# Optimization experiments

Hardware: AMD Instinct MI355X
Metric: run time of the kernel (lower is better)

## Reference

```python
import jax, jax.numpy as jnp
import numpy as np
import math

B, L, I, H = 32, 2048, 64, 512
HALF = H // 2
DT = 0.05
RHO = 0.99
INPUT_SCALING = 1.0
STD = 1.0
GAMMA_MIN, GAMMA_MAX = 0.5, 1.0
EPS_MIN, EPS_MAX = 0.5, 1.0


def setup_inputs() -> dict:
    key = jax.random.key(0)
    ks = jax.random.split(key, 7)
    x = jax.random.normal(ks[0], (B, L, I), dtype=jnp.float32)
    x2h = jax.random.uniform(ks[1], (I, H), dtype=jnp.float32) * INPUT_SCALING
    h2h = 2.0 * (2.0 * jax.random.uniform(ks[2], (H, H), dtype=jnp.float32) - 1.0)
    # spectral_norm_scaling: rescale so largest singular value == rho
    h2h = h2h * (RHO / jnp.linalg.norm(h2h, ord=2))
    bias = (2.0 * jax.random.uniform(ks[3], (H,), dtype=jnp.float32) - 1.0) * INPUT_SCALING
    gamma = jax.random.uniform(ks[4], (H,), dtype=jnp.float32) * (GAMMA_MAX - GAMMA_MIN) + GAMMA_MIN
    epsilon = jax.random.uniform(ks[5], (H,), dtype=jnp.float32) * (EPS_MAX - EPS_MIN) + EPS_MIN
    # RandomFourierFeature: W_sin = W_cos, shape [half_dim, in_dim]
    W_rff = jax.random.normal(ks[6], (HALF, H), dtype=jnp.float32) * STD
    return {"x": x, "x2h": x2h, "h2h": h2h, "bias": bias,
            "gamma": gamma, "epsilon": epsilon, "W_rff": W_rff}


def _run(x, x2h, h2h, bias, gamma, epsilon, W_rff):
    b = x.shape[0]
    inv_sqrt_half = 1.0 / math.sqrt(HALF)

    def step(carry, xt):
        hy, hz, zsum = carry
        pre = jnp.tanh(xt @ x2h + hy @ h2h + bias)          # [B,H]
        hz = hz + DT * (pre - gamma * hy - epsilon * hz)
        hy = hy + DT * hz
        wx = hy @ W_rff.T                                   # [B,HALF]
        z = jnp.concatenate([jnp.cos(wx), jnp.sin(wx)], axis=-1) * inv_sqrt_half
        return (hy, hz, zsum + z), None

    hy0 = jnp.zeros((b, H), dtype=x.dtype)
    hz0 = jnp.zeros((b, H), dtype=x.dtype)
    zsum0 = jnp.zeros((b, H), dtype=x.dtype)
    (hy, hz, zsum), _ = jax.lax.scan(step, (hy0, hz0, zsum0), jnp.swapaxes(x, 0, 1))
    mu = zsum / x.shape[1]  # mean over time of per-step RFF states
    return mu, hy


def reference(x, x2h, h2h, bias, gamma, epsilon, W_rff):
    return _run(x, x2h, h2h, bias, gamma, epsilon, W_rff)
```

## Files before the change

### kernel.cpp

```cpp
#include <hip/hip_runtime.h>
#include <math.h>

#define Bz 32
#define Lz 2048
#define Iz 64
#define Hz 512
#define HALFz 256
#define DTz 0.05f
#define NMEM 8
#define TPB 512

#define FMA4(P, S, W) do { (P).x = fmaf((S), (W).x, (P).x); (P).y = fmaf((S), (W).y, (P).y); \
                           (P).z = fmaf((S), (W).z, (P).z); (P).w = fmaf((S), (W).w, (P).w); } while(0)

__global__ __launch_bounds__(TPB, 2) void coesn_l2(
    const float* __restrict__ x, const float* __restrict__ x2h,
    const float* __restrict__ h2h, const float* __restrict__ bias,
    const float* __restrict__ gam, const float* __restrict__ eps,
    const float* __restrict__ W_rff, unsigned long long* __restrict__ gbuf,
    float* __restrict__ out) {
  __shared__ __align__(16) float hyf[2][Hz];
  __shared__ __align__(16) float xb[2][Iz];
  __shared__ __align__(16) float part[NMEM][64];

  const int b    = blockIdx.x & 31;
  const int m    = blockIdx.x >> 5;
  const int u    = threadIdx.x;
  const int c0   = m * 64;
  const int ksl  = u >> 4;
  const int cg   = u & 15;
  const int wv   = u >> 6;
  const int lane = u & 63;
  const int rloc = u >> 4;
  const int kseg = u & 15;

  float4 wreg[16];
  #pragma unroll
  for (int k = 0; k < 16; ++k)
    wreg[k] = *(const float4*)(h2h + (size_t)(ksl * 16 + k) * Hz + c0 + 4 * cg);
  float4 xreg[2];
  #pragma unroll
  for (int j = 0; j < 2; ++j)
    xreg[j] = *(const float4*)(x2h + (size_t)(ksl * 2 + j) * Hz + c0 + 4 * cg);
  float wr[32];
  {
    const float* wp = W_rff + (size_t)(m * 32 + rloc) * Hz + kseg * 32;
    #pragma unroll
    for (int j = 0; j < 32; ++j) wr[j] = wp[j];
  }

  float hy = 0.f, hz = 0.f, bu = 0.f, gu = 0.f, eu = 0.f;
  if (u < 64) { bu = bias[c0 + u]; gu = gam[c0 + u]; eu = eps[c0 + u]; }
  hyf[0][u] = 0.f;
  if (u < 16) ((float4*)xb[0])[u] = ((const float4*)(x + (size_t)b * Lz * Iz))[u];
  float zc = 0.f, zs = 0.f;
  __syncthreads();

  auto rff_acc = [&](const float* hsrc) {
    float acc = 0.f;
    #pragma unroll
    for (int i = 0; i < 8; ++i) {
      int q = kseg * 8 + i;
      float4 h4 = ((const float4*)hsrc)[q ^ ((q >> 3) & 7)];
      acc = fmaf(h4.x, wr[4 * i], acc);
      acc = fmaf(h4.y, wr[4 * i + 1], acc);
      acc = fmaf(h4.z, wr[4 * i + 2], acc);
      acc = fmaf(h4.w, wr[4 * i + 3], acc);
    }
    acc += __shfl_xor(acc, 1); acc += __shfl_xor(acc, 2);
    acc += __shfl_xor(acc, 4); acc += __shfl_xor(acc, 8);
    float sv, cv;
    __sincosf(acc, &sv, &cv);
    zc += cv; zs += sv;
  };

  for (int t = 0; t < Lz; ++t) {
    const int cur = t & 1, nxt = cur ^ 1;

    float hv[16];
    #pragma unroll
    for (int j = 0; j < 4; ++j) {
      int q = ksl * 4 + j;
      float4 h4 = ((const float4*)hyf[cur])[q ^ ((q >> 3) & 7)];
      hv[4 * j] = h4.x; hv[4 * j + 1] = h4.y; hv[4 * j + 2] = h4.z; hv[4 * j + 3] = h4.w;
    }
    float4 p = make_float4(0.f, 0.f, 0.f, 0.f);
    #pragma unroll
    for (int k = 0; k < 16; ++k) FMA4(p, hv[k], wreg[k]);
    {
      const float* xcur = xb[cur];
      FMA4(p, xcur[ksl * 2], xreg[0]);
      FMA4(p, xcur[ksl * 2 + 1], xreg[1]);
    }
    if (u < 16 && t + 1 < Lz)
      ((float4*)xb[nxt])[u] =
          ((const float4*)(x + ((size_t)b * Lz + (t + 1)) * Iz))[u];
    p.x += __shfl_xor(p.x, 16); p.y += __shfl_xor(p.y, 16);
    p.z += __shfl_xor(p.z, 16); p.w += __shfl_xor(p.w, 16);
    p.x += __shfl_xor(p.x, 32); p.y += __shfl_xor(p.y, 32);
    p.z += __shfl_xor(p.z, 32); p.w += __shfl_xor(p.w, 32);
    if (lane < 16) ((float4*)part[wv])[lane] = p;
    __syncthreads();

    const unsigned tag = (unsigned)(t + 1);
    unsigned long long* A = gbuf + ((size_t)nxt * Bz + b) * Hz;

    if (u < 64) {
      float s = 0.f;
      #pragma unroll
      for (int w = 0; w < 8; ++w) s += part[w][u];
      s += bu;
      float e2 = __expf(s + s);
      float pre = 1.f - 2.f * __builtin_amdgcn_rcpf(e2 + 1.f);
      float hzn = fmaf(DTz, pre - gu * hy - eu * hz, hz);
      hy = fmaf(DTz, hzn, hy);
      hz = hzn;
      unsigned bits = __float_as_uint(hy);
      unsigned ax = (bits & 0xffff0000u) | tag;
      unsigned ay = (bits << 16) | tag;
      *(volatile unsigned long long*)(A + c0 + u) =
          ((unsigned long long)ay << 32) | ax;
      unsigned* Bd = (unsigned*)(A + c0 + u);
      __hip_atomic_store(Bd, ax, __ATOMIC_RELAXED, __HIP_MEMORY_SCOPE_AGENT);
      __hip_atomic_store(Bd + 1, ay, __ATOMIC_RELAXED, __HIP_MEMORY_SCOPE_AGENT);
      int q = (c0 + u) >> 2;
      hyf[nxt][(q ^ ((q >> 3) & 7)) * 4 + (u & 3)] = hy;
    }

    if (t > 0) rff_acc(hyf[cur]);

    if (wv != m) {
      unsigned ax, ay; int it = 0;
      for (;;) {
        unsigned long long v = *(volatile const unsigned long long*)(A + u);
        ax = (unsigned)v; ay = (unsigned)(v >> 32);
        if (!(((ax ^ tag) | (ay ^ tag)) & 0xffffu)) break;
        if (it >= 4) {
          const unsigned* Bd = (const unsigned*)(A + u);
          ax = __hip_atomic_load(Bd, __ATOMIC_RELAXED, __HIP_MEMORY_SCOPE_AGENT);
          ay = __hip_atomic_load(Bd + 1, __ATOMIC_RELAXED, __HIP_MEMORY_SCOPE_AGENT);
          if (!(((ax ^ tag) | (ay ^ tag)) & 0xffffu)) break;
        }
        if (++it > (1 << 20)) break;
      }
      int q = u >> 2;
      hyf[nxt][(q ^ ((q >> 3) & 7)) * 4 + (u & 3)] =
          __uint_as_float((ax & 0xffff0000u) | (ay >> 16));
    }
    __syncthreads();
  }

  rff_acc(hyf[0]);

  if (u < 64) out[(size_t)Bz * Hz + (size_t)b * Hz + c0 + u] = hy;
  if (kseg == 0) {
    const float sc = 0.0625f / 2048.f;
    out[(size_t)b * Hz + m * 32 + rloc] = zc * sc;
    out[(size_t)b * Hz + HALFz + m * 32 + rloc] = zs * sc;
  }
}

__global__ __launch_bounds__(512) void coesn_scan_fb(
    const float* __restrict__ x, const float* __restrict__ x2h,
    const float* __restrict__ h2h, const float* __restrict__ bias,
    const float* __restrict__ gam, const float* __restrict__ eps,
    const float* __restrict__ W_rff, float* __restrict__ out) {
  const int b = blockIdx.x;
  const int u = threadIdx.x;
  __shared__ __align__(16) float hy_lds[Hz];
  __shared__ __align__(16) float x_lds[Iz];
  __shared__ float4 part[4][128];
  __shared__ float wx_lds[HALFz];

  float hy = 0.f, hz = 0.f, zsum = 0.f;
  const float bu = bias[u];
  const float gu = gam[u];
  const float eu = eps[u];

  const int kq = u >> 7;
  const int g  = u & 127;
  const int jj = u >> 2;
  const int ks = u & 3;

  const float4* __restrict__ H4 = (const float4*)h2h;
  const float4* __restrict__ X2 = (const float4*)x2h;
  const float4* __restrict__ W4 = (const float4*)W_rff;
  const float4* __restrict__ XG = (const float4*)x;
  const float4* hy4 = (const float4*)hy_lds;

  hy_lds[u] = 0.f;
  if (u < 16) ((float4*)x_lds)[u] = XG[(long)b * Lz * 16 + u];
  __syncthreads();

  for (int t = 0; t < Lz; ++t) {
    float4 p = make_float4(0.f, 0.f, 0.f, 0.f);
    {
      const float4* hp = (const float4*)&hy_lds[kq << 7];
      #pragma unroll 8
      for (int k4 = 0; k4 < 32; ++k4) {
        float4 hv = hp[k4];
        const float4* wr2 = &H4[(size_t)((kq << 7) + (k4 << 2)) * 128 + g];
        float4 w0 = wr2[0]; float4 w1 = wr2[128]; float4 w2 = wr2[256]; float4 w3 = wr2[384];
        FMA4(p, hv.x, w0); FMA4(p, hv.y, w1); FMA4(p, hv.z, w2); FMA4(p, hv.w, w3);
      }
      const float4* xp = (const float4*)&x_lds[kq << 4];
      #pragma unroll
      for (int k4 = 0; k4 < 4; ++k4) {
        float4 xv = xp[k4];
        const float4* wr2 = &X2[(size_t)((kq << 4) + (k4 << 2)) * 128 + g];
        float4 w0 = wr2[0]; float4 w1 = wr2[128]; float4 w2 = wr2[256]; float4 w3 = wr2[384];
        FMA4(p, xv.x, w0); FMA4(p, xv.y, w1); FMA4(p, xv.z, w2); FMA4(p, xv.w, w3);
      }
    }
    part[kq][g] = p;
    __syncthreads();
    {
      const float* pp = (const float*)part;
      float s = (pp[u] + pp[512 + u]) + (pp[1024 + u] + pp[1536 + u]);
      float pre = tanhf(s + bu);
      float hzn = fmaf(DTz, pre - gu * hy - eu * hz, hz);
      hy = fmaf(DTz, hzn, hy);
      hz = hzn;
      hy_lds[u] = hy;
      if (u < 16 && t + 1 < Lz)
        ((float4*)x_lds)[u] = XG[((long)b * Lz + (t + 1)) * 16 + u];
    }
    __syncthreads();
    {
      float4 acc0 = make_float4(0.f,0.f,0.f,0.f), acc1 = make_float4(0.f,0.f,0.f,0.f);
      #pragma unroll 4
      for (int it = 0; it < 32; ++it) {
        int k4 = (it << 2) + ks;
        float4 hv = hy4[k4];
        float4 w0 = W4[(size_t)jj * 128 + k4];
        float4 w1 = W4[(size_t)(jj + 128) * 128 + k4];
        acc0.x = fmaf(hv.x, w0.x, acc0.x); acc0.y = fmaf(hv.y, w0.y, acc0.y);
        acc0.z = fmaf(hv.z, w0.z, acc0.z); acc0.w = fmaf(hv.w, w0.w, acc0.w);
        acc1.x = fmaf(hv.x, w1.x, acc1.x); acc1.y = fmaf(hv.y, w1.y, acc1.y);
        acc1.z = fmaf(hv.z, w1.z, acc1.z); acc1.w = fmaf(hv.w, w1.w, acc1.w);
      }
      float a0 = (acc0.x + acc0.y) + (acc0.z + acc0.w);
      float a1 = (acc1.x + acc1.y) + (acc1.z + acc1.w);
      a0 += __shfl_xor(a0, 1); a0 += __shfl_xor(a0, 2);
      a1 += __shfl_xor(a1, 1); a1 += __shfl_xor(a1, 2);
      if (ks == 0) { wx_lds[jj] = a0; wx_lds[jj + 128] = a1; }
    }
    __syncthreads();
    {
      float v = wx_lds[u & 255];
      zsum += (u < HALFz) ? cosf(v) : sinf(v);
    }
  }
  out[(long)b * Hz + u] = zsum * (0.0625f / 2048.f);
  out[(long)Bz * Hz + (long)b * Hz + u] = hy;
}

extern "C" void kernel_launch(void* const* d_in, const int* in_sizes, int n_in,
                              void* d_out, int out_size, void* d_ws, size_t ws_size,
                              hipStream_t stream) {
  const float* x    = (const float*)d_in[0];
  const float* x2h  = (const float*)d_in[1];
  const float* h2h  = (const float*)d_in[2];
  const float* bias = (const float*)d_in[3];
  const float* gam  = (const float*)d_in[4];
  const float* eps  = (const float*)d_in[5];
  const float* wrff = (const float*)d_in[6];
  float* out = (float*)d_out;

  const size_t WS_NEED = (size_t)2 * Bz * Hz * sizeof(unsigned long long);
  if (ws_size >= WS_NEED) {
    unsigned long long* gbuf = (unsigned long long*)d_ws;
    hipMemsetAsync(d_ws, 0, WS_NEED, stream);
    void* args[] = { (void*)&x, (void*)&x2h, (void*)&h2h, (void*)&bias,
                     (void*)&gam, (void*)&eps, (void*)&wrff,
                     (void*)&gbuf, (void*)&out };
    hipError_t e = hipLaunchCooperativeKernel((const void*)coesn_l2,
                                              dim3(Bz * NMEM), dim3(TPB),
                                              args, 0, stream);
    if (e == hipSuccess) return;
  }
  coesn_scan_fb<<<Bz, 512, 0, stream>>>(x, x2h, h2h, bias, gam, eps, wrff, out);
}
```

Baseline: 4.264 ms.

## Reduce matvec within each wave and drop the intra-step block barrier

The per-step hy@h2h matvec is remapped so that each wave owns 8 output columns and each lane covers 8 rows. The reduction now runs entirely with butterfly shuffles inside the wave, which removes the shared-memory partial buffer and one __syncthreads per timestep. The cross-block exchange changes to a single 64-bit packed tagged word, written to two separate buffers: a volatile copy and an atomic copy. The fallback to atomic loads now starts after two spins instead of four. In exchange, every wave computes the tanh/update redundantly across lanes and holds a 64-float weight register tile, and the exchange needs a workspace twice as large.

New measurement: 3.412 ms. 1.25x faster.

```diff
diff --git a/kernel.cpp b/kernel.cpp
--- a/kernel.cpp
+++ b/kernel.cpp
@@ -10,58 +10,78 @@
 #define NMEM 8
 #define TPB 512
 
-#define FMA4(P, S, W) do { (P).x = fmaf((S), (W).x, (P).x); (P).y = fmaf((S), (W).y, (P).y); \
-                           (P).z = fmaf((S), (W).z, (P).z); (P).w = fmaf((S), (W).w, (P).w); } while(0)
-
-__global__ __launch_bounds__(TPB, 2) void coesn_l2(
+typedef unsigned long long u64;
+
+__device__ __forceinline__ bool tagok(u64 v, unsigned tag) {
+  u64 want = (u64)tag | ((u64)tag << 48);
+  return ((v ^ want) & 0xFFFF00000000FFFFull) == 0ull;
+}
+__device__ __forceinline__ u64 packv(float f, unsigned tag) {
+  return (u64)tag | ((u64)__float_as_uint(f) << 16) | ((u64)tag << 48);
+}
+__device__ __forceinline__ float unpackv(u64 v) {
+  return __uint_as_float((unsigned)(v >> 16));
+}
+
+__global__ __launch_bounds__(TPB, 2) void coesn_x2(
     const float* __restrict__ x, const float* __restrict__ x2h,
     const float* __restrict__ h2h, const float* __restrict__ bias,
     const float* __restrict__ gam, const float* __restrict__ eps,
-    const float* __restrict__ W_rff, unsigned long long* __restrict__ gbuf,
-    float* __restrict__ out) {
+    const float* __restrict__ W_rff, u64* __restrict__ Xb,
+    u64* __restrict__ Yb, float* __restrict__ out) {
   __shared__ __align__(16) float hyf[2][Hz];
   __shared__ __align__(16) float xb[2][Iz];
-  __shared__ __align__(16) float part[NMEM][64];
-
-  const int b    = blockIdx.x & 31;
-  const int m    = blockIdx.x >> 5;
-  const int u    = threadIdx.x;
-  const int c0   = m * 64;
-  const int ksl  = u >> 4;
-  const int cg   = u & 15;
-  const int wv   = u >> 6;
-  const int lane = u & 63;
-  const int rloc = u >> 4;
-  const int kseg = u & 15;
-
-  float4 wreg[16];
-  #pragma unroll
-  for (int k = 0; k < 16; ++k)
-    wreg[k] = *(const float4*)(h2h + (size_t)(ksl * 16 + k) * Hz + c0 + 4 * cg);
-  float4 xreg[2];
-  #pragma unroll
-  for (int j = 0; j < 2; ++j)
-    xreg[j] = *(const float4*)(x2h + (size_t)(ksl * 2 + j) * Hz + c0 + 4 * cg);
+
+  const int b  = blockIdx.x & 31;
+  const int m  = blockIdx.x >> 5;
+  const int u  = threadIdx.x;
+  const int w  = u >> 6;
+  const int l  = u & 63;
+  const int c0 = m * 64;
+  const int j  = ((l & 1) << 2) | (l & 2) | ((l >> 2) & 1);
+  const int mycol = c0 + w * 8 + j;
+  const int rloc = u >> 4, kseg = u & 15;
+
+  float wreg[8][8];
+  {
+    const float* hrow = h2h + (size_t)(8 * l) * Hz + c0 + 8 * w;
+    #pragma unroll
+    for (int r = 0; r < 8; ++r) {
+      float4 v0 = *(const float4*)(hrow + (size_t)r * Hz);
+      float4 v1 = *(const float4*)(hrow + (size_t)r * Hz + 4);
+      wreg[r][0] = v0.x; wreg[r][1] = v0.y; wreg[r][2] = v0.z; wreg[r][3] = v0.w;
+      wreg[r][4] = v1.x; wreg[r][5] = v1.y; wreg[r][6] = v1.z; wreg[r][7] = v1.w;
+    }
+  }
+  float xreg[8];
+  {
+    float4 v0 = *(const float4*)(x2h + (size_t)l * Hz + c0 + 8 * w);
+    float4 v1 = *(const float4*)(x2h + (size_t)l * Hz + c0 + 8 * w + 4);
+    xreg[0] = v0.x; xreg[1] = v0.y; xreg[2] = v0.z; xreg[3] = v0.w;
+    xreg[4] = v1.x; xreg[5] = v1.y; xreg[6] = v1.z; xreg[7] = v1.w;
+  }
   float wr[32];
   {
     const float* wp = W_rff + (size_t)(m * 32 + rloc) * Hz + kseg * 32;
     #pragma unroll
-    for (int j = 0; j < 32; ++j) wr[j] = wp[j];
-  }
-
-  float hy = 0.f, hz = 0.f, bu = 0.f, gu = 0.f, eu = 0.f;
-  if (u < 64) { bu = bias[c0 + u]; gu = gam[c0 + u]; eu = eps[c0 + u]; }
+    for (int i = 0; i < 32; ++i) wr[i] = wp[i];
+  }
+
+  const float bu = bias[mycol];
+  const float gu = gam[mycol];
+  const float eu = eps[mycol];
+  float hy = 0.f, hz = 0.f, zc = 0.f, zs = 0.f;
   hyf[0][u] = 0.f;
   if (u < 16) ((float4*)xb[0])[u] = ((const float4*)(x + (size_t)b * Lz * Iz))[u];
-  float zc = 0.f, zs = 0.f;
   __syncthreads();
 
   auto rff_acc = [&](const float* hsrc) {
     float acc = 0.f;
+    const float4* hp = (const float4*)hsrc;
     #pragma unroll
     for (int i = 0; i < 8; ++i) {
       int q = kseg * 8 + i;
-      float4 h4 = ((const float4*)hsrc)[q ^ ((q >> 3) & 7)];
+      float4 h4 = hp[q ^ ((q >> 3) & 7)];
       acc = fmaf(h4.x, wr[4 * i], acc);
       acc = fmaf(h4.y, wr[4 * i + 1], acc);
       acc = fmaf(h4.z, wr[4 * i + 2], acc);
@@ -77,88 +97,103 @@
   for (int t = 0; t < Lz; ++t) {
     const int cur = t & 1, nxt = cur ^ 1;
 
-    float hv[16];
-    #pragma unroll
-    for (int j = 0; j < 4; ++j) {
-      int q = ksl * 4 + j;
-      float4 h4 = ((const float4*)hyf[cur])[q ^ ((q >> 3) & 7)];
-      hv[4 * j] = h4.x; hv[4 * j + 1] = h4.y; hv[4 * j + 2] = h4.z; hv[4 * j + 3] = h4.w;
-    }
-    float4 p = make_float4(0.f, 0.f, 0.f, 0.f);
-    #pragma unroll
-    for (int k = 0; k < 16; ++k) FMA4(p, hv[k], wreg[k]);
-    {
-      const float* xcur = xb[cur];
-      FMA4(p, xcur[ksl * 2], xreg[0]);
-      FMA4(p, xcur[ksl * 2 + 1], xreg[1]);
-    }
     if (u < 16 && t + 1 < Lz)
       ((float4*)xb[nxt])[u] =
           ((const float4*)(x + ((size_t)b * Lz + (t + 1)) * Iz))[u];
-    p.x += __shfl_xor(p.x, 16); p.y += __shfl_xor(p.y, 16);
-    p.z += __shfl_xor(p.z, 16); p.w += __shfl_xor(p.w, 16);
-    p.x += __shfl_xor(p.x, 32); p.y += __shfl_xor(p.y, 32);
-    p.z += __shfl_xor(p.z, 32); p.w += __shfl_xor(p.w, 32);
-    if (lane < 16) ((float4*)part[wv])[lane] = p;
-    __syncthreads();
+
+    float hv[8];
+    {
+      const float4* hp = (const float4*)hyf[cur];
+      int q0 = 2 * l, q1 = 2 * l + 1;
+      float4 h0 = hp[q0 ^ ((q0 >> 3) & 7)];
+      float4 h1 = hp[q1 ^ ((q1 >> 3) & 7)];
+      hv[0] = h0.x; hv[1] = h0.y; hv[2] = h0.z; hv[3] = h0.w;
+      hv[4] = h1.x; hv[5] = h1.y; hv[6] = h1.z; hv[7] = h1.w;
+    }
+    float a[8] = {0.f, 0.f, 0.f, 0.f, 0.f, 0.f, 0.f, 0.f};
+    #pragma unroll
+    for (int r = 0; r < 8; ++r) {
+      float h = hv[r];
+      #pragma unroll
+      for (int c = 0; c < 8; ++c) a[c] = fmaf(h, wreg[r][c], a[c]);
+    }
+    {
+      float xv = xb[cur][l];
+      #pragma unroll
+      for (int c = 0; c < 8; ++c) a[c] = fmaf(xv, xreg[c], a[c]);
+    }
+    #pragma unroll
+    for (int i = 0; i < 4; ++i) {
+      float snd = (l & 1) ? a[i] : a[i + 4];
+      float rcv = __shfl_xor(snd, 1);
+      a[i] = ((l & 1) ? a[i + 4] : a[i]) + rcv;
+    }
+    #pragma unroll
+    for (int i = 0; i < 2; ++i) {
+      float snd = (l & 2) ? a[i] : a[i + 2];
+      float rcv = __shfl_xor(snd, 2);
+      a[i] = ((l & 2) ? a[i + 2] : a[i]) + rcv;
+    }
+    float s;
+    {
+      float snd = (l & 4) ? a[0] : a[1];
+      float rcv = __shfl_xor(snd, 4);
+      s = ((l & 4) ? a[1] : a[0]) + rcv;
+    }
+    s += __shfl_xor(s, 8); s += __shfl_xor(s, 16); s += __shfl_xor(s, 32);
+
+    s += bu;
+    float e2 = __expf(s + s);
+    float pre = 1.f - 2.f * __builtin_amdgcn_rcpf(e2 + 1.f);
+    float hzn = fmaf(DTz, pre - gu * hy - eu * hz, hz);
+    hy = fmaf(DTz, hzn, hy);
+    hz = hzn;
 
     const unsigned tag = (unsigned)(t + 1);
-    unsigned long long* A = gbuf + ((size_t)nxt * Bz + b) * Hz;
-
-    if (u < 64) {
-      float s = 0.f;
-      #pragma unroll
-      for (int w = 0; w < 8; ++w) s += part[w][u];
-      s += bu;
-      float e2 = __expf(s + s);
-      float pre = 1.f - 2.f * __builtin_amdgcn_rcpf(e2 + 1.f);
-      float hzn = fmaf(DTz, pre - gu * hy - eu * hz, hz);
-      hy = fmaf(DTz, hzn, hy);
-      hz = hzn;
-      unsigned bits = __float_as_uint(hy);
-      unsigned ax = (bits & 0xffff0000u) | tag;
-      unsigned ay = (bits << 16) | tag;
-      *(volatile unsigned long long*)(A + c0 + u) =
-          ((unsigned long long)ay << 32) | ax;
-      unsigned* Bd = (unsigned*)(A + c0 + u);
-      __hip_atomic_store(Bd, ax, __ATOMIC_RELAXED, __HIP_MEMORY_SCOPE_AGENT);
-      __hip_atomic_store(Bd + 1, ay, __ATOMIC_RELAXED, __HIP_MEMORY_SCOPE_AGENT);
-      int q = (c0 + u) >> 2;
-      hyf[nxt][(q ^ ((q >> 3) & 7)) * 4 + (u & 3)] = hy;
+    u64* XA = Xb + ((size_t)nxt * Bz + b) * Hz;
+    u64* YA = Yb + ((size_t)nxt * Bz + b) * Hz;
+
+    if (l < 8) {
+      u64 pv = packv(hy, tag);
+      *(volatile u64*)(XA + mycol) = pv;
+      __hip_atomic_store(YA + mycol, pv, __ATOMIC_RELAXED,
+                         __HIP_MEMORY_SCOPE_AGENT);
+      int q = mycol >> 2;
+      hyf[nxt][(q ^ ((q >> 3) & 7)) * 4 + (mycol & 3)] = hy;
     }
 
     if (t > 0) rff_acc(hyf[cur]);
 
-    if (wv != m) {
-      unsigned ax, ay; int it = 0;
+    if (w != m) {
+      u64 v; int it = 0;
       for (;;) {
-        unsigned long long v = *(volatile const unsigned long long*)(A + u);
-        ax = (unsigned)v; ay = (unsigned)(v >> 32);
-        if (!(((ax ^ tag) | (ay ^ tag)) & 0xffffu)) break;
-        if (it >= 4) {
-          const unsigned* Bd = (const unsigned*)(A + u);
-          ax = __hip_atomic_load(Bd, __ATOMIC_RELAXED, __HIP_MEMORY_SCOPE_AGENT);
-          ay = __hip_atomic_load(Bd + 1, __ATOMIC_RELAXED, __HIP_MEMORY_SCOPE_AGENT);
-          if (!(((ax ^ tag) | (ay ^ tag)) & 0xffffu)) break;
+        v = *(volatile const u64*)(XA + u);
+        if (tagok(v, tag)) break;
+        if (it >= 2) {
+          v = __hip_atomic_load(YA + u, __ATOMIC_RELAXED,
+                                __HIP_MEMORY_SCOPE_AGENT);
+          if (tagok(v, tag)) break;
         }
         if (++it > (1 << 20)) break;
       }
       int q = u >> 2;
-      hyf[nxt][(q ^ ((q >> 3) & 7)) * 4 + (u & 3)] =
-          __uint_as_float((ax & 0xffff0000u) | (ay >> 16));
+      hyf[nxt][(q ^ ((q >> 3) & 7)) * 4 + (u & 3)] = unpackv(v);
     }
     __syncthreads();
   }
 
   rff_acc(hyf[0]);
 
-  if (u < 64) out[(size_t)Bz * Hz + (size_t)b * Hz + c0 + u] = hy;
+  if (l < 8) out[(size_t)Bz * Hz + (size_t)b * Hz + mycol] = hy;
   if (kseg == 0) {
     const float sc = 0.0625f / 2048.f;
     out[(size_t)b * Hz + m * 32 + rloc] = zc * sc;
     out[(size_t)b * Hz + HALFz + m * 32 + rloc] = zs * sc;
   }
 }
+
+#define FMA4(P, S, W) do { (P).x = fmaf((S), (W).x, (P).x); (P).y = fmaf((S), (W).y, (P).y); \
+                           (P).z = fmaf((S), (W).z, (P).z); (P).w = fmaf((S), (W).w, (P).w); } while(0)
 
 __global__ __launch_bounds__(512) void coesn_scan_fb(
     const float* __restrict__ x, const float* __restrict__ x2h,
@@ -267,14 +302,16 @@
   const float* wrff = (const float*)d_in[6];
   float* out = (float*)d_out;
 
-  const size_t WS_NEED = (size_t)2 * Bz * Hz * sizeof(unsigned long long);
+  const size_t NEX = (size_t)2 * Bz * Hz;
+  const size_t WS_NEED = 2 * NEX * sizeof(u64);
   if (ws_size >= WS_NEED) {
-    unsigned long long* gbuf = (unsigned long long*)d_ws;
+    u64* Xb = (u64*)d_ws;
+    u64* Yb = Xb + NEX;
     hipMemsetAsync(d_ws, 0, WS_NEED, stream);
     void* args[] = { (void*)&x, (void*)&x2h, (void*)&h2h, (void*)&bias,
                      (void*)&gam, (void*)&eps, (void*)&wrff,
-                     (void*)&gbuf, (void*)&out };
-    hipError_t e = hipLaunchCooperativeKernel((const void*)coesn_l2,
+                     (void*)&Xb, (void*)&Yb, (void*)&out };
+    hipError_t e = hipLaunchCooperativeKernel((const void*)coesn_x2,
                                               dim3(Bz * NMEM), dim3(TPB),
                                               args, 0, stream);
     if (e == hipSuccess) return;
```
